# Optimization experiments

Hardware: AMD Instinct MI355X
Metric: run time of the kernel (lower is better)

Reference implementation:

```python
import jax, jax.numpy as jnp
import numpy as np

B, H, W, C = 4, 64, 64, 32
M1 = M2 = 16
N = H * W          # 4096 grid nodes per sample
E = 131072         # edges (avg degree 32)
EDIM = 6           # edge feature dim
KMID = 64          # kernel MLP hidden width
EPS = 1e-5         # InstanceNorm eps


def _gelu(x):
    return jax.nn.gelu(x, approximate=False)  # torch nn.GELU default is exact erf


def _mlp(x, w1, b1, w2, b2):
    return _gelu(x @ w1 + b1) @ w2 + b2


def _inorm(x):
    # torch InstanceNorm2d(affine=False) applied to [B,H,W,C]: normalizes over last two dims
    m = x.mean(axis=(2, 3), keepdims=True)
    v = x.var(axis=(2, 3), keepdims=True)
    return (x - m) * jax.lax.rsqrt(v + EPS)


def _lin_init(k, fin, fout):
    lim = 1.0 / np.sqrt(fin)
    kw, kb = jax.random.split(k)
    w = jax.random.uniform(kw, (fin, fout), jnp.float32, -lim, lim)
    b = jax.random.uniform(kb, (fout,), jnp.float32, -lim, lim)
    return w, b


def setup_inputs() -> dict:
    key = jax.random.key(0)
    ks = jax.random.split(key, 14)
    s = 1.0 / (C * C)
    inp = {}
    inp['nodes'] = jax.random.normal(ks[0], (B, H, W, C), jnp.float32)
    inp['edge_index'] = jax.random.randint(ks[1], (2, E), 0, N, dtype=jnp.int64)
    inp['edge_attr'] = jax.random.uniform(ks[2], (E, EDIM), jnp.float32)
    # spectral conv complex weights, stored as real/imag float32 pairs
    inp['w1_re'] = s * jax.random.uniform(ks[3], (C, C, M1, M2), jnp.float32)
    inp['w1_im'] = s * jax.random.uniform(ks[4], (C, C, M1, M2), jnp.float32)
    inp['w2_re'] = s * jax.random.uniform(ks[5], (C, C, M1, M2), jnp.float32)
    inp['w2_im'] = s * jax.random.uniform(ks[6], (C, C, M1, M2), jnp.float32)
    # self.mlp : MLP(C, C, 2C)
    inp['mlp_w1'], inp['mlp_b1'] = _lin_init(ks[7], C, 2 * C)
    inp['mlp_w2'], inp['mlp_b2'] = _lin_init(ks[8], 2 * C, C)
    # self.w : MLP(C, C, 2C)
    inp['wm_w1'], inp['wm_b1'] = _lin_init(ks[9], C, 2 * C)
    inp['wm_w2'], inp['wm_b2'] = _lin_init(ks[10], 2 * C, C)
    # GNO kernel MLP : EDIM -> KMID -> C*C
    inp['ker_w1'], inp['ker_b1'] = _lin_init(ks[11], EDIM, KMID)
    inp['ker_w2'], inp['ker_b2'] = _lin_init(ks[12], KMID, C * C)
    # NNConv root weight and bias (PyG uniform(size) init with size=in_channels)
    lim = 1.0 / np.sqrt(C)
    kr, kb = jax.random.split(ks[13])
    inp['root'] = jax.random.uniform(kr, (C, C), jnp.float32, -lim, lim)
    inp['gbias'] = jax.random.uniform(kb, (C,), jnp.float32, -lim, lim)
    return inp


def reference(nodes, edge_index, edge_attr, w1_re, w1_im, w2_re, w2_im,
              mlp_w1, mlp_b1, mlp_w2, mlp_b2, wm_w1, wm_b1, wm_w2, wm_b2,
              ker_w1, ker_b1, ker_w2, ker_b2, root, gbias):
    x = _inorm(nodes)                                             # [B,H,W,C]

    # --- spectral conv branch ---
    x_ft = jnp.fft.rfftn(x, axes=(1, 2), norm='ortho')            # [B,H,W//2+1,C]
    w1 = (w1_re + 1j * w1_im).astype(jnp.complex64)
    w2 = (w2_re + 1j * w2_im).astype(jnp.complex64)
    top = jnp.einsum('bxyi,ioxy->bxyo', x_ft[:, :M1, :M2, :], w1)
    bot = jnp.einsum('bxyi,ioxy->bxyo', x_ft[:, -M1:, :M2, :], w2)
    out_ft = jnp.zeros((B, H, W // 2 + 1, C), jnp.complex64)
    out_ft = out_ft.at[:, :M1, :M2, :].set(top).at[:, -M1:, :M2, :].set(bot)
    x1 = jnp.fft.irfftn(out_ft, axes=(1, 2), s=(H, W), norm='ortho')
    x1 = _mlp(_inorm(x1), mlp_w1, mlp_b1, mlp_w2, mlp_b2)         # [B,H,W,C]

    # --- pointwise MLP branch ---
    x2 = _inorm(_mlp(x, wm_w1, wm_b1, wm_w2, wm_b2))              # [B,H,W,C]

    # --- edge-conditioned GNO branch ---
    x3 = x.reshape(B, N, C)
    wmat = _mlp(edge_attr, ker_w1, ker_b1, ker_w2, ker_b2).reshape(E, C, C)
    src, dst = edge_index[0], edge_index[1]
    msg = jnp.einsum('bec,eco->beo', x3[:, src, :], wmat)         # [B,E,C]
    agg = jnp.zeros((B, N, C), jnp.float32).at[:, dst, :].add(msg)
    x3 = agg + x3 @ root + gbias                                  # [B,N,C]

    return _gelu(x1 + x2 + x3.reshape(B, H, W, C))
```

## Files before the change

kernel.cpp:

```cpp
#include <hip/hip_runtime.h>

#define E_ 131072

typedef _Float16 half8 __attribute__((ext_vector_type(8)));
typedef float f32x4 __attribute__((ext_vector_type(4)));

__device__ __forceinline__ float gelu_f(float x) {
    return 0.5f * x * (1.0f + erff(x * 0.70710678118654752f));
}

#define TWOPI_64 (6.2831853071795864769f / 64.0f)

__device__ __forceinline__ void block_reduce2(float& s, float& s2, float* red) {
    #pragma unroll
    for (int off = 32; off > 0; off >>= 1) {
        s  += __shfl_down(s, off, 64);
        s2 += __shfl_down(s2, off, 64);
    }
    int lane = threadIdx.x & 63, wv = threadIdx.x >> 6;
    __syncthreads();
    if (lane == 0) { red[wv] = s; red[wv + 4] = s2; }
    __syncthreads();
    s  = red[0] + red[1] + red[2] + red[3];
    s2 = red[4] + red[5] + red[6] + red[7];
}

__device__ __forceinline__ void gno_body(int e0, float* sbufF, float* sB2, int* ssrc, int* sdst,
                                         const float* __restrict__ ea,
                                         const float* __restrict__ kw1, const float* __restrict__ kb1,
                                         const float* __restrict__ kb2,
                                         const _Float16* __restrict__ whi, const _Float16* __restrict__ wlo,
                                         const float* __restrict__ xn, const int* __restrict__ ei,
                                         float* __restrict__ agg) {
    _Float16* sxTh = (_Float16*)sbufF;
    int t = threadIdx.x;
    int lane = t & 63, wv = t >> 6, quad = lane >> 4, l15 = lane & 15;
    int eg = wv >> 1, t2 = wv & 1;

    if (t < 64) ssrc[t] = ei[e0 + t];
    else if (t < 128) sdst[t - 64] = ei[E_ + e0 + t - 64];
    for (int f = t; f < 1024; f += 256) sB2[f] = kb2[f];
    {
        int r = t >> 2, k0 = (t & 3) * 16;
        const float* ep = ea + (e0 + r) * 6;
        float e6[6];
        #pragma unroll
        for (int d = 0; d < 6; ++d) e6[d] = ep[d];
        #pragma unroll
        for (int kk = 0; kk < 16; ++kk) {
            int k = k0 + kk;
            float acc = kb1[k];
            #pragma unroll
            for (int d = 0; d < 6; ++d) acc += e6[d] * kw1[d * 64 + k];
            sbufF[r * 68 + k] = gelu_f(acc);
        }
    }
    __syncthreads();
    half8 ahi[2][2], alo[2][2];
    #pragma unroll
    for (int et = 0; et < 2; ++et) {
        #pragma unroll
        for (int kh = 0; kh < 2; ++kh) {
            const float* hp = sbufF + (eg * 32 + et * 16 + l15) * 68 + kh * 32 + quad * 8;
            float4 h0 = *(const float4*)hp;
            float4 h1 = *(const float4*)(hp + 4);
            float hv[8] = {h0.x, h0.y, h0.z, h0.w, h1.x, h1.y, h1.z, h1.w};
            half8 hh, hl;
            #pragma unroll
            for (int j = 0; j < 8; ++j) {
                _Float16 hi = (_Float16)hv[j];
                hh[j] = hi;
                hl[j] = (_Float16)(hv[j] - (float)hi);
            }
            ahi[et][kh] = hh;
            alo[et][kh] = hl;
        }
    }
    __syncthreads();
    {
        int b = t & 3, r = t >> 2;
        int s = ssrc[r];
        int pe = (r >> 5) * 32 + ((r >> 2) & 3) * 8 + ((r >> 4) & 1) * 4 + (r & 3);
        const float4* xp = (const float4*)(xn + (b * 4096 + s) * 32);
        _Float16* dp = sxTh + b * 2312 + pe;
        #pragma unroll
        for (int q = 0; q < 8; ++q) {
            float4 v = xp[q];
            dp[(q * 4 + 0) * 72] = (_Float16)v.x;
            dp[(q * 4 + 1) * 72] = (_Float16)v.y;
            dp[(q * 4 + 2) * 72] = (_Float16)v.z;
            dp[(q * 4 + 3) * 72] = (_Float16)v.w;
        }
    }
    __syncthreads();
    float msg[4][2][4];
    #pragma unroll
    for (int b = 0; b < 4; ++b)
        #pragma unroll
        for (int et = 0; et < 2; ++et)
            #pragma unroll
            for (int r = 0; r < 4; ++r) msg[b][et][r] = 0.f;

    for (int i = 0; i < 32; ++i) {
        float b2v = sB2[i * 32 + t2 * 16 + l15];
        int f0 = (i * 4 + t2 * 2) * 512 + lane * 8;
        half8 bhi0 = *(const half8*)(whi + f0);
        half8 bhi1 = *(const half8*)(whi + f0 + 512);
        half8 blo0 = *(const half8*)(wlo + f0);
        half8 blo1 = *(const half8*)(wlo + f0 + 512);
        f32x4 acc[2];
        #pragma unroll
        for (int et = 0; et < 2; ++et) {
            f32x4 ac = {b2v, b2v, b2v, b2v};
            ac = __builtin_amdgcn_mfma_f32_16x16x32_f16(ahi[et][0], bhi0, ac, 0, 0, 0);
            ac = __builtin_amdgcn_mfma_f32_16x16x32_f16(ahi[et][1], bhi1, ac, 0, 0, 0);
            ac = __builtin_amdgcn_mfma_f32_16x16x32_f16(ahi[et][0], blo0, ac, 0, 0, 0);
            ac = __builtin_amdgcn_mfma_f32_16x16x32_f16(ahi[et][1], blo1, ac, 0, 0, 0);
            ac = __builtin_amdgcn_mfma_f32_16x16x32_f16(alo[et][0], bhi0, ac, 0, 0, 0);
            ac = __builtin_amdgcn_mfma_f32_16x16x32_f16(alo[et][1], bhi1, ac, 0, 0, 0);
            acc[et] = ac;
        }
        #pragma unroll
        for (int b = 0; b < 4; ++b) {
            const half8 xv = *(const half8*)(sxTh + b * 2312 + i * 72 + eg * 32 + quad * 8);
            #pragma unroll
            for (int et = 0; et < 2; ++et) {
                msg[b][et][0] += (float)xv[et * 4 + 0] * acc[et][0];
                msg[b][et][1] += (float)xv[et * 4 + 1] * acc[et][1];
                msg[b][et][2] += (float)xv[et * 4 + 2] * acc[et][2];
                msg[b][et][3] += (float)xv[et * 4 + 3] * acc[et][3];
            }
        }
    }
    int o = t2 * 16 + l15;
    #pragma unroll
    for (int et = 0; et < 2; ++et) {
        #pragma unroll
        for (int r = 0; r < 4; ++r) {
            int row = eg * 32 + et * 16 + quad * 4 + r;
            int d = sdst[row];
            #pragma unroll
            for (int b = 0; b < 4; ++b) {
                atomicAdd(&agg[(b * 4096 + d) * 32 + o], msg[b][et][r]);
            }
        }
    }
}

__global__ __launch_bounds__(256, 4) void k_pre(const float* __restrict__ nodes,
                                                const float* __restrict__ w2,
                                                float* __restrict__ xn,
                                                float* __restrict__ agg,
                                                float* __restrict__ Gre, float* __restrict__ Gim,
                                                _Float16* __restrict__ whi, _Float16* __restrict__ wlo) {
    int t = threadIdx.x;
    if (blockIdx.x >= 256) {
        int g0 = (blockIdx.x - 256) * 512 + t;
        #pragma unroll 1
        for (int rep = 0; rep < 2; ++rep) {
            int g = g0 + rep * 256;
            int j = g & 7, l = (g >> 3) & 63, fid = g >> 9;
            int i = fid >> 2, t2 = (fid >> 1) & 1, kh = fid & 1;
            int quad = l >> 4, l15 = l & 15;
            int k = kh * 32 + quad * 8 + j;
            int n = i * 32 + t2 * 16 + l15;
            float v = w2[k * 1024 + n];
            _Float16 hi = (_Float16)v;
            whi[g] = hi;
            wlo[g] = (_Float16)(v - (float)hi);
        }
        return;
    }
    int bh = blockIdx.x;
    __shared__ float sx[2048];
    __shared__ float tc[64], ts[64];
    __shared__ float red[8];
    const float4* src = (const float4*)(nodes + bh * 2048);
    float4* dst = (float4*)(xn + bh * 2048);
    float4* az = (float4*)(agg + bh * 2048);
    if (t < 64) { float a = TWOPI_64 * t; tc[t] = cosf(a); ts[t] = sinf(a); }
    float4 v0 = src[t * 2], v1 = src[t * 2 + 1];
    float s  = v0.x + v0.y + v0.z + v0.w + v1.x + v1.y + v1.z + v1.w;
    float s2 = v0.x*v0.x + v0.y*v0.y + v0.z*v0.z + v0.w*v0.w
             + v1.x*v1.x + v1.y*v1.y + v1.z*v1.z + v1.w*v1.w;
    block_reduce2(s, s2, red);
    float mean = s * (1.0f / 2048.0f);
    float var  = s2 * (1.0f / 2048.0f) - mean * mean;
    float sc = rsqrtf(var + 1e-5f);
    v0.x = (v0.x - mean) * sc; v0.y = (v0.y - mean) * sc;
    v0.z = (v0.z - mean) * sc; v0.w = (v0.w - mean) * sc;
    v1.x = (v1.x - mean) * sc; v1.y = (v1.y - mean) * sc;
    v1.z = (v1.z - mean) * sc; v1.w = (v1.w - mean) * sc;
    dst[t * 2] = v0; dst[t * 2 + 1] = v1;
    float4 z = {0.f, 0.f, 0.f, 0.f};
    az[t * 2] = z; az[t * 2 + 1] = z;
    ((float4*)sx)[t * 2] = v0;
    ((float4*)sx)[t * 2 + 1] = v1;
    __syncthreads();
    #pragma unroll 1
    for (int rep = 0; rep < 2; ++rep) {
        int oi = rep * 256 + t;
        int ky = oi >> 5, i = oi & 31;
        float re = 0.f, im = 0.f;
        #pragma unroll 8
        for (int w = 0; w < 64; ++w) {
            float v = sx[w * 32 + i];
            int m = (ky * w) & 63;
            re += v * tc[m];
            im -= v * ts[m];
        }
        Gre[bh * 512 + oi] = re;
        Gim[bh * 512 + oi] = im;
    }
}

__global__ __launch_bounds__(256, 4) void k_g1(
        const float* __restrict__ Gre, const float* __restrict__ Gim,
        const float* __restrict__ w1re, const float* __restrict__ w1im,
        const float* __restrict__ w2re, const float* __restrict__ w2im,
        float* __restrict__ Yr, float* __restrict__ Yi,
        const float* __restrict__ ea,
        const float* __restrict__ kw1, const float* __restrict__ kb1,
        const float* __restrict__ kb2,
        const _Float16* __restrict__ whi, const _Float16* __restrict__ wlo,
        const float* __restrict__ xn,
        const int* __restrict__ ei,
        float* __restrict__ agg) {
    __shared__ __align__(16) float U[5648];
    __shared__ int ssrc[64], sdst[64];
    int t = threadIdx.x;

    if (blockIdx.x < 128) {
        float* tc  = U;
        float* ts  = U + 64;
        float* sXr = U + 128;
        float* sXi = U + 656;
        int bid = blockIdx.x;
        int b = bid >> 5, kxi = bid & 31;
        int kx = kxi + (kxi < 16 ? 0 : 32);
        int x = kxi & 15;
        const float* wre = (kxi < 16) ? w1re : w2re;
        const float* wim = (kxi < 16) ? w1im : w2im;
        if (t < 64) { float a = TWOPI_64 * t; tc[t] = cosf(a); ts[t] = sinf(a); }
        __syncthreads();
        #pragma unroll 1
        for (int rep = 0; rep < 2; ++rep) {
            int oi = rep * 256 + t;
            int ky = oi >> 5, i = oi & 31;
            float re = 0.f, im = 0.f;
            #pragma unroll 8
            for (int h = 0; h < 64; ++h) {
                int gidx = (b * 64 + h) * 512 + ky * 32 + i;
                float gr = Gre[gidx], gi = Gim[gidx];
                int m = (kx * h) & 63;
                float c = tc[m], sv = ts[m];
                re += gr * c + gi * sv;
                im += gi * c - gr * sv;
            }
            sXr[ky * 33 + i] = re;
            sXi[ky * 33 + i] = im;
        }
        __syncthreads();
        #pragma unroll 1
        for (int rep = 0; rep < 2; ++rep) {
            int oi = rep * 256 + t;
            int ky = oi & 15, o = oi >> 4;
            float re = 0.f, im = 0.f;
            #pragma unroll 4
            for (int i = 0; i < 32; ++i) {
                float xr = sXr[ky * 33 + i], xi = sXi[ky * 33 + i];
                int widx = (i * 32 + o) * 256 + x * 16 + ky;
                float wr = wre[widx], wi = wim[widx];
                re += xr * wr - xi * wi;
                im += xr * wi + xi * wr;
            }
            Yr[bid * 512 + ky * 32 + o] = re;
            Yi[bid * 512 + ky * 32 + o] = im;
        }
        return;
    }
    gno_body((blockIdx.x - 128) * 64, U, U + 4624, ssrc, sdst,
             ea, kw1, kb1, kb2, whi, wlo, xn, ei, agg);
}

__global__ __launch_bounds__(256, 4) void k_g2(
        const float* __restrict__ Yr, const float* __restrict__ Yi,
        const float* __restrict__ mw1, const float* __restrict__ mb1,
        const float* __restrict__ mw2, const float* __restrict__ mb2,
        float* __restrict__ osum,
        const float* __restrict__ ea,
        const float* __restrict__ kw1, const float* __restrict__ kb1,
        const float* __restrict__ kb2,
        const _Float16* __restrict__ whi, const _Float16* __restrict__ wlo,
        const float* __restrict__ xn,
        const int* __restrict__ ei,
        float* __restrict__ agg) {
    __shared__ __align__(16) float U[11584];
    __shared__ int ssrc[64], sdst[64];
    int t = threadIdx.x;

    if (blockIdx.x < 256) {
        int bh = blockIdx.x;
        int b = bh >> 6, h = bh & 63;
        float* tc  = U;
        float* ts  = U + 64;
        float* red = U + 128;
        float* sZr = U + 136;
        float* sZi = U + 664;
        float* sP  = U + 1192;
        float* sW1 = U + 3304;
        float* sW2 = U + 5352;
        float* sH  = U + 7400;
        if (t < 64) { float a = TWOPI_64 * t; tc[t] = cosf(a); ts[t] = sinf(a); }
        for (int f = t; f < 2048; f += 256) { sW1[f] = mw1[f]; sW2[f] = mw2[f]; }
        __syncthreads();
        #pragma unroll 1
        for (int rep = 0; rep < 2; ++rep) {
            int oi = rep * 256 + t;
            int ky = oi >> 5, o = oi & 31;
            float re = 0.f, im = 0.f;
            #pragma unroll 4
            for (int kxi = 0; kxi < 32; ++kxi) {
                int kx = kxi + (kxi < 16 ? 0 : 32);
                int m = (kx * h) & 63;
                float c = tc[m], sv = ts[m];
                int yidx = (b * 32 + kxi) * 512 + ky * 32 + o;
                float yr = Yr[yidx], yi = Yi[yidx];
                re += yr * c - yi * sv;
                im += yr * sv + yi * c;
            }
            sZr[ky * 33 + o] = re;
            sZi[ky * 33 + o] = im;
        }
        __syncthreads();
        float s = 0.f, s2 = 0.f;
        #pragma unroll 1
        for (int rep = 0; rep < 8; ++rep) {
            int idx = rep * 256 + t;
            int w = idx >> 5, o = idx & 31;
            float acc = sZr[o];
            #pragma unroll
            for (int ky = 1; ky < 16; ++ky) {
                int m = (ky * w) & 63;
                acc += 2.0f * (sZr[ky * 33 + o] * tc[m] - sZi[ky * 33 + o] * ts[m]);
            }
            acc *= (1.0f / 4096.0f);
            sP[w * 33 + o] = acc;
            s += acc; s2 += acc * acc;
        }
        block_reduce2(s, s2, red);
        float mean = s * (1.0f / 2048.0f);
        float sc = rsqrtf(s2 * (1.0f / 2048.0f) - mean * mean + 1e-5f);
        #pragma unroll 1
        for (int rep = 0; rep < 8; ++rep) {
            int idx = rep * 256 + t;
            int w = idx >> 5, o = idx & 31;
            sP[w * 33 + o] = (sP[w * 33 + o] - mean) * sc;
        }
        __syncthreads();
        #pragma unroll 1
        for (int rep = 0; rep < 16; ++rep) {
            int idx = rep * 256 + t;
            int w = idx >> 6, k = idx & 63;
            float acc = mb1[k];
            #pragma unroll 4
            for (int c = 0; c < 32; ++c) acc += sP[w * 33 + c] * sW1[c * 64 + k];
            sH[w * 65 + k] = gelu_f(acc);
        }
        __syncthreads();
        #pragma unroll 1
        for (int rep = 0; rep < 8; ++rep) {
            int idx = rep * 256 + t;
            int w = idx >> 5, o = idx & 31;
            float acc = mb2[o];
            #pragma unroll 4
            for (int k = 0; k < 64; ++k) acc += sH[w * 65 + k] * sW2[k * 32 + o];
            osum[bh * 2048 + idx] = acc;
        }
        return;
    }
    gno_body((1408 + blockIdx.x - 256) * 64, U, U + 4624, ssrc, sdst,
             ea, kw1, kb1, kb2, whi, wlo, xn, ei, agg);
}

__global__ __launch_bounds__(256, 2) void k_final2(const float* __restrict__ osum, const float* __restrict__ agg,
                                                   const float* __restrict__ xn,
                                                   const float* __restrict__ ww1, const float* __restrict__ wb1,
                                                   const float* __restrict__ ww2, const float* __restrict__ wb2,
                                                   const float* __restrict__ root, const float* __restrict__ gbias,
                                                   float* __restrict__ out) {
    int bh = blockIdx.x;
    int t = threadIdx.x;
    __shared__ float red[8];
    __shared__ float sX[2112];
    __shared__ float sH[4160];
    __shared__ float sW1[2048], sW2[2048];
    __shared__ float sR[1024];
    __shared__ float sP[2112];
    for (int f = t; f < 2048; f += 256) {
        sW1[f] = ww1[f]; sW2[f] = ww2[f];
        sX[(f >> 5) * 33 + (f & 31)] = xn[bh * 2048 + f];
    }
    for (int f = t; f < 1024; f += 256) sR[f] = root[f];
    __syncthreads();
    #pragma unroll 1
    for (int rep = 0; rep < 16; ++rep) {
        int idx = rep * 256 + t;
        int w = idx >> 6, k = idx & 63;
        float acc = wb1[k];
        #pragma unroll 4
        for (int c = 0; c < 32; ++c) acc += sX[w * 33 + c] * sW1[c * 64 + k];
        sH[w * 65 + k] = gelu_f(acc);
    }
    __syncthreads();
    float s = 0.f, s2 = 0.f;
    #pragma unroll 1
    for (int rep = 0; rep < 8; ++rep) {
        int idx = rep * 256 + t;
        int w = idx >> 5, o = idx & 31;
        float acc = wb2[o];
        #pragma unroll 4
        for (int k = 0; k < 64; ++k) acc += sH[w * 65 + k] * sW2[k * 32 + o];
        sP[w * 33 + o] = acc;
        s += acc; s2 += acc * acc;
    }
    block_reduce2(s, s2, red);
    float mean = s * (1.0f / 2048.0f);
    float sc = rsqrtf(s2 * (1.0f / 2048.0f) - mean * mean + 1e-5f);
    #pragma unroll 1
    for (int rep = 0; rep < 8; ++rep) {
        int idx = rep * 256 + t;
        int w = idx >> 5, o = idx & 31;
        float acc = gbias[o] + osum[bh * 2048 + idx] + agg[bh * 2048 + idx]
                  + (sP[w * 33 + o] - mean) * sc;
        #pragma unroll 4
        for (int c = 0; c < 32; ++c) acc += sX[w * 33 + c] * sR[c * 32 + o];
        out[bh * 2048 + idx] = gelu_f(acc);
    }
}

extern "C" void kernel_launch(void* const* d_in, const int* in_sizes, int n_in,
                              void* d_out, int out_size, void* d_ws, size_t ws_size,
                              hipStream_t stream) {
    (void)in_sizes; (void)n_in; (void)out_size; (void)ws_size;
    const float* nodes  = (const float*)d_in[0];
    const int*   eidx   = (const int*)d_in[1];
    const float* eattr  = (const float*)d_in[2];
    const float* w1re   = (const float*)d_in[3];
    const float* w1im   = (const float*)d_in[4];
    const float* w2re   = (const float*)d_in[5];
    const float* w2im   = (const float*)d_in[6];
    const float* mlp_w1 = (const float*)d_in[7];
    const float* mlp_b1 = (const float*)d_in[8];
    const float* mlp_w2 = (const float*)d_in[9];
    const float* mlp_b2 = (const float*)d_in[10];
    const float* wm_w1  = (const float*)d_in[11];
    const float* wm_b1  = (const float*)d_in[12];
    const float* wm_w2  = (const float*)d_in[13];
    const float* wm_b2  = (const float*)d_in[14];
    const float* ker_w1 = (const float*)d_in[15];
    const float* ker_b1 = (const float*)d_in[16];
    const float* ker_w2 = (const float*)d_in[17];
    const float* ker_b2 = (const float*)d_in[18];
    const float* root   = (const float*)d_in[19];
    const float* gbias  = (const float*)d_in[20];
    float* out = (float*)d_out;

    char* ws = (char*)d_ws;
    size_t off = 0;
    auto alloc = [&](size_t bytes) {
        void* p = ws + off;
        off += (bytes + 255) & ~(size_t)255;
        return p;
    };
    float* xn   = (float*)alloc(524288 * 4);
    float* agg  = (float*)alloc(524288 * 4);
    float* osum = (float*)alloc(524288 * 4);
    float* Gre  = (float*)alloc(131072 * 4);
    float* Gim  = (float*)alloc(131072 * 4);
    float* Yr   = (float*)alloc(65536 * 4);
    float* Yi   = (float*)alloc(65536 * 4);
    _Float16* whi = (_Float16*)alloc(65536 * 2);
    _Float16* wlo = (_Float16*)alloc(65536 * 2);

    k_pre<<<384, 256, 0, stream>>>(nodes, ker_w2, xn, agg, Gre, Gim, whi, wlo);
    k_g1<<<1536, 256, 0, stream>>>(Gre, Gim, w1re, w1im, w2re, w2im, Yr, Yi,
                                   eattr, ker_w1, ker_b1, ker_b2, whi, wlo, xn, eidx, agg);
    k_g2<<<896, 256, 0, stream>>>(Yr, Yi, mlp_w1, mlp_b1, mlp_w2, mlp_b2, osum,
                                  eattr, ker_w1, ker_b1, ker_b2, whi, wlo, xn, eidx, agg);
    k_final2<<<256, 256, 0, stream>>>(osum, agg, xn, wm_w1, wm_b1, wm_w2, wm_b2, root, gbias, out);
}
```

Before: 256.2 us.

## Move pointwise MLP+InstanceNorm branch into k_pre and rebalance GNO edge blocks

```diff
diff --git a/kernel.cpp b/kernel.cpp
--- a/kernel.cpp
+++ b/kernel.cpp
@@ -149,8 +149,11 @@
 
 __global__ __launch_bounds__(256, 4) void k_pre(const float* __restrict__ nodes,
                                                 const float* __restrict__ w2,
+                                                const float* __restrict__ ww1, const float* __restrict__ wb1,
+                                                const float* __restrict__ ww2, const float* __restrict__ wb2,
                                                 float* __restrict__ xn,
                                                 float* __restrict__ agg,
+                                                float* __restrict__ osum,
                                                 float* __restrict__ Gre, float* __restrict__ Gim,
                                                 _Float16* __restrict__ whi, _Float16* __restrict__ wlo) {
     int t = threadIdx.x;
@@ -172,13 +175,16 @@
         return;
     }
     int bh = blockIdx.x;
-    __shared__ float sx[2048];
+    __shared__ float sx[2112];
     __shared__ float tc[64], ts[64];
     __shared__ float red[8];
+    __shared__ float sW1[2048], sW2[2048];
+    __shared__ float sH[4160];
     const float4* src = (const float4*)(nodes + bh * 2048);
     float4* dst = (float4*)(xn + bh * 2048);
     float4* az = (float4*)(agg + bh * 2048);
     if (t < 64) { float a = TWOPI_64 * t; tc[t] = cosf(a); ts[t] = sinf(a); }
+    for (int f = t; f < 2048; f += 256) { sW1[f] = ww1[f]; sW2[f] = ww2[f]; }
     float4 v0 = src[t * 2], v1 = src[t * 2 + 1];
     float s  = v0.x + v0.y + v0.z + v0.w + v1.x + v1.y + v1.z + v1.w;
     float s2 = v0.x*v0.x + v0.y*v0.y + v0.z*v0.z + v0.w*v0.w
@@ -194,8 +200,12 @@
     dst[t * 2] = v0; dst[t * 2 + 1] = v1;
     float4 z = {0.f, 0.f, 0.f, 0.f};
     az[t * 2] = z; az[t * 2 + 1] = z;
-    ((float4*)sx)[t * 2] = v0;
-    ((float4*)sx)[t * 2 + 1] = v1;
+    {
+        int w = t >> 2, c0 = (t & 3) * 8;
+        float* p = sx + w * 33 + c0;
+        p[0] = v0.x; p[1] = v0.y; p[2] = v0.z; p[3] = v0.w;
+        p[4] = v1.x; p[5] = v1.y; p[6] = v1.z; p[7] = v1.w;
+    }
     __syncthreads();
     #pragma unroll 1
     for (int rep = 0; rep < 2; ++rep) {
@@ -204,13 +214,43 @@
         float re = 0.f, im = 0.f;
         #pragma unroll 8
         for (int w = 0; w < 64; ++w) {
-            float v = sx[w * 32 + i];
+            float v = sx[w * 33 + i];
             int m = (ky * w) & 63;
             re += v * tc[m];
             im -= v * ts[m];
         }
         Gre[bh * 512 + oi] = re;
         Gim[bh * 512 + oi] = im;
+    }
+    __syncthreads();
+    #pragma unroll 1
+    for (int rep = 0; rep < 16; ++rep) {
+        int idx = rep * 256 + t;
+        int w = idx >> 6, k = idx & 63;
+        float acc = wb1[k];
+        #pragma unroll 4
+        for (int c = 0; c < 32; ++c) acc += sx[w * 33 + c] * sW1[c * 64 + k];
+        sH[w * 65 + k] = gelu_f(acc);
+    }
+    __syncthreads();
+    s = 0.f; s2 = 0.f;
+    #pragma unroll 1
+    for (int rep = 0; rep < 8; ++rep) {
+        int idx = rep * 256 + t;
+        int w = idx >> 5, o = idx & 31;
+        float acc = wb2[o];
+        #pragma unroll 4
+        for (int k = 0; k < 64; ++k) acc += sH[w * 65 + k] * sW2[k * 32 + o];
+        sW1[idx] = acc;
+        s += acc; s2 += acc * acc;
+    }
+    block_reduce2(s, s2, red);
+    mean = s * (1.0f / 2048.0f);
+    sc = rsqrtf(s2 * (1.0f / 2048.0f) - mean * mean + 1e-5f);
+    #pragma unroll 1
+    for (int rep = 0; rep < 8; ++rep) {
+        int idx = rep * 256 + t;
+        osum[bh * 2048 + idx] = (sW1[idx] - mean) * sc;
     }
 }
 
@@ -375,67 +415,33 @@
             float acc = mb2[o];
             #pragma unroll 4
             for (int k = 0; k < 64; ++k) acc += sH[w * 65 + k] * sW2[k * 32 + o];
-            osum[bh * 2048 + idx] = acc;
+            osum[bh * 2048 + idx] += acc;
         }
         return;
     }
-    gno_body((1408 + blockIdx.x - 256) * 64, U, U + 4624, ssrc, sdst,
+    gno_body((1152 + blockIdx.x - 256) * 64, U, U + 4624, ssrc, sdst,
              ea, kw1, kb1, kb2, whi, wlo, xn, ei, agg);
 }
 
-__global__ __launch_bounds__(256, 2) void k_final2(const float* __restrict__ osum, const float* __restrict__ agg,
-                                                   const float* __restrict__ xn,
-                                                   const float* __restrict__ ww1, const float* __restrict__ wb1,
-                                                   const float* __restrict__ ww2, const float* __restrict__ wb2,
-                                                   const float* __restrict__ root, const float* __restrict__ gbias,
-                                                   float* __restrict__ out) {
-    int bh = blockIdx.x;
+__global__ __launch_bounds__(256, 4) void k_final(const float* __restrict__ osum, const float* __restrict__ agg,
+                                                  const float* __restrict__ xn, const float* __restrict__ root,
+                                                  const float* __restrict__ gbias, float* __restrict__ out) {
+    int bh = blockIdx.x >> 2, q = blockIdx.x & 3;
+    int base = bh * 2048 + q * 512;
     int t = threadIdx.x;
-    __shared__ float red[8];
-    __shared__ float sX[2112];
-    __shared__ float sH[4160];
-    __shared__ float sW1[2048], sW2[2048];
+    __shared__ float sX[16 * 33];
     __shared__ float sR[1024];
-    __shared__ float sP[2112];
-    for (int f = t; f < 2048; f += 256) {
-        sW1[f] = ww1[f]; sW2[f] = ww2[f];
-        sX[(f >> 5) * 33 + (f & 31)] = xn[bh * 2048 + f];
-    }
+    for (int f = t; f < 512; f += 256) sX[(f >> 5) * 33 + (f & 31)] = xn[base + f];
     for (int f = t; f < 1024; f += 256) sR[f] = root[f];
     __syncthreads();
     #pragma unroll 1
-    for (int rep = 0; rep < 16; ++rep) {
-        int idx = rep * 256 + t;
-        int w = idx >> 6, k = idx & 63;
-        float acc = wb1[k];
-        #pragma unroll 4
-        for (int c = 0; c < 32; ++c) acc += sX[w * 33 + c] * sW1[c * 64 + k];
-        sH[w * 65 + k] = gelu_f(acc);
-    }
-    __syncthreads();
-    float s = 0.f, s2 = 0.f;
-    #pragma unroll 1
-    for (int rep = 0; rep < 8; ++rep) {
+    for (int rep = 0; rep < 2; ++rep) {
         int idx = rep * 256 + t;
         int w = idx >> 5, o = idx & 31;
-        float acc = wb2[o];
-        #pragma unroll 4
-        for (int k = 0; k < 64; ++k) acc += sH[w * 65 + k] * sW2[k * 32 + o];
-        sP[w * 33 + o] = acc;
-        s += acc; s2 += acc * acc;
-    }
-    block_reduce2(s, s2, red);
-    float mean = s * (1.0f / 2048.0f);
-    float sc = rsqrtf(s2 * (1.0f / 2048.0f) - mean * mean + 1e-5f);
-    #pragma unroll 1
-    for (int rep = 0; rep < 8; ++rep) {
-        int idx = rep * 256 + t;
-        int w = idx >> 5, o = idx & 31;
-        float acc = gbias[o] + osum[bh * 2048 + idx] + agg[bh * 2048 + idx]
-                  + (sP[w * 33 + o] - mean) * sc;
+        float acc = gbias[o] + osum[base + idx] + agg[base + idx];
         #pragma unroll 4
         for (int c = 0; c < 32; ++c) acc += sX[w * 33 + c] * sR[c * 32 + o];
-        out[bh * 2048 + idx] = gelu_f(acc);
+        out[base + idx] = gelu_f(acc);
     }
 }
 
@@ -483,10 +489,11 @@
     _Float16* whi = (_Float16*)alloc(65536 * 2);
     _Float16* wlo = (_Float16*)alloc(65536 * 2);
 
-    k_pre<<<384, 256, 0, stream>>>(nodes, ker_w2, xn, agg, Gre, Gim, whi, wlo);
-    k_g1<<<1536, 256, 0, stream>>>(Gre, Gim, w1re, w1im, w2re, w2im, Yr, Yi,
+    k_pre<<<384, 256, 0, stream>>>(nodes, ker_w2, wm_w1, wm_b1, wm_w2, wm_b2,
+                                   xn, agg, osum, Gre, Gim, whi, wlo);
+    k_g1<<<1280, 256, 0, stream>>>(Gre, Gim, w1re, w1im, w2re, w2im, Yr, Yi,
                                    eattr, ker_w1, ker_b1, ker_b2, whi, wlo, xn, eidx, agg);
-    k_g2<<<896, 256, 0, stream>>>(Yr, Yi, mlp_w1, mlp_b1, mlp_w2, mlp_b2, osum,
-                                  eattr, ker_w1, ker_b1, ker_b2, whi, wlo, xn, eidx, agg);
-    k_final2<<<256, 256, 0, stream>>>(osum, agg, xn, wm_w1, wm_b1, wm_w2, wm_b2, root, gbias, out);
-}
+    k_g2<<<1152, 256, 0, stream>>>(Yr, Yi, mlp_w1, mlp_b1, mlp_w2, mlp_b2, osum,
+                                   eattr, ker_w1, ker_b1, ker_b2, whi, wlo, xn, eidx, agg);
+    k_final<<<1024, 256, 0, stream>>>(osum, agg, xn, root, gbias, out);
+}
```

Result: no change. 254.4 us (-0.7%).
